# Performance work log

Measured on AMD Instinct MI355X. Metric: run time of the kernel, lower is better.

Reference implementation:

```python
import jax, jax.numpy as jnp
import numpy as np


def setup_inputs() -> dict:
    key = jax.random.key(0)
    k_x, k_pos, k_val, k_temp = jax.random.split(key, 4)
    B, T, D, N = 8, 2048, 512, 4096
    x = jax.random.normal(k_x, (B, T, D), dtype=jnp.float32)
    # module init: positions ~ N(0,1)*0.5, values ~ N(0,1)*0.02
    positions = jax.random.normal(k_pos, (N, D), dtype=jnp.float32) * 0.5
    values = jax.random.normal(k_val, (N, D), dtype=jnp.float32) * 0.02
    # 'trained' temperatures ~ U[4,6] so the RBF kernel does not underflow at D=512
    temperature = 4.0 + 2.0 * jax.random.uniform(k_temp, (N,), dtype=jnp.float32)
    # neuron_scale buffer at late-tide level (MAX_SCALE = 0.8)
    neuron_scale = jnp.full((N,), 0.8, dtype=jnp.float32)
    return {"x": x, "positions": positions, "values": values,
            "temperature": temperature, "neuron_scale": neuron_scale}


def reference(x, positions, values, temperature, neuron_scale):
    B, T, D = x.shape
    x_flat = x.reshape(-1, D)                                  # [M, D], M = B*T
    x_sq = jnp.sum(x_flat * x_flat, axis=-1, keepdims=True)    # [M, 1]
    p_sq = jnp.sum(positions * positions, axis=-1)             # [N]
    cross = x_flat @ positions.T                               # [M, N] GEMM
    dists = jnp.sqrt(jnp.maximum(x_sq + p_sq[None, :] - 2.0 * cross, 0.0))
    effective_temp = (jnp.abs(temperature) + 0.1) * neuron_scale  # [N]
    weights = jnp.exp(-dists / effective_temp[None, :])        # [M, N]
    weights = weights / (jnp.sum(weights, axis=-1, keepdims=True) + 1e-8)
    out = weights @ values                                     # [M, D] GEMM
    return out.reshape(B, T, D)
```

## Files before the change

kernel.cpp:

```cpp
#include <hip/hip_runtime.h>
#include <hip/hip_bf16.h>

typedef __attribute__((ext_vector_type(8))) short short8;
typedef __attribute__((ext_vector_type(4))) float f32x4;
typedef __attribute__((ext_vector_type(4))) unsigned short u16x4;

__device__ __forceinline__ unsigned short f2bf(float f) {
  union { float f; unsigned u; } v; v.f = f;
  unsigned r = v.u + 0x7fffu + ((v.u >> 16) & 1u);
  return (unsigned short)(r >> 16);
}

template <int EPI, int WM, int WN, int MI, int BK, int NBUF>
__global__ __launch_bounds__(512, 4) void rbf_gemm(
    const unsigned short* __restrict__ A, const unsigned short* __restrict__ Bt,
    int Ncols, int K,
    const float* __restrict__ xsq, const float* __restrict__ psq,
    const float* __restrict__ rtemp, unsigned short* __restrict__ Wout,
    float* __restrict__ part, int Mtot, const float* __restrict__ denin,
    float* __restrict__ outp, int row0, int ldOut) {
  constexpr int BM = WM * MI * 16;
  constexpr int BN = WN * 64;
  constexpr int CH = BK / 8;
  constexpr int CMASK = CH - 1;
  constexpr int AIT = BM * CH / 512;
  constexpr int BIT = BN * CH / 512;
  constexpr int LOADS = AIT + BIT;
  constexpr int DEPTH = NBUF - 1;
  constexpr int KS = BK / 32;
  constexpr int ASZ = BM * BK;
  constexpr int TSZ = (BM + BN) * BK;
  constexpr int BOUNCE = EPI == 1 ? BM * BN * 2 : BM * BN;
  constexpr int SELEMS = NBUF * TSZ > BOUNCE ? NBUF * TSZ : BOUNCE;
  __shared__ __align__(16) unsigned short smem[SELEMS];

  const int t = threadIdx.x;
  const int lane = t & 63, wid = t >> 6;
  const int wm = wid / WN, wn = wid % WN;
  const int lr = lane & 15, lg = lane >> 4;

  const int nb = Ncols / BN;
  const int nwg = gridDim.x;
  int swz = blockIdx.x;
  if ((nwg & 7) == 0) {
    int cpx = nwg >> 3;
    swz = (swz & 7) * cpx + (swz >> 3);
  }
  const int bm = swz / nb, bn = swz - bm * nb;

  const unsigned short* Ab = A + (size_t)bm * BM * K;
  const unsigned short* Bb = Bt + (size_t)bn * BN * K;

  const unsigned short* gA[AIT];
  const unsigned short* gB[BIT];
#pragma unroll
  for (int i = 0; i < AIT; ++i) {
    const int idx = i * 512 + t;
    const int r = idx / CH, c = idx & CMASK;
    gA[i] = Ab + (size_t)r * K + ((c ^ (r & CMASK)) << 3);
  }
#pragma unroll
  for (int i = 0; i < BIT; ++i) {
    const int idx = i * 512 + t;
    const int r = idx / CH, c = idx & CMASK;
    gB[i] = Bb + (size_t)r * K + ((c ^ (r & CMASK)) << 3);
  }
  const int dwave = wid << 9;

  int offA[MI][KS], offB[4][KS];
#pragma unroll
  for (int mi = 0; mi < MI; ++mi) {
    const int ar = wm * (MI * 16) + mi * 16 + lr;
#pragma unroll
    for (int ks = 0; ks < KS; ++ks)
      offA[mi][ks] = ar * BK + ((((ks << 2) | lg) ^ (ar & CMASK)) << 3);
  }
#pragma unroll
  for (int ni = 0; ni < 4; ++ni) {
    const int br = wn * 64 + ni * 16 + lr;
#pragma unroll
    for (int ks = 0; ks < KS; ++ks)
      offB[ni][ks] = ASZ + br * BK + ((((ks << 2) | lg) ^ (br & CMASK)) << 3);
  }

  f32x4 acc[MI][4];
#pragma unroll
  for (int i = 0; i < MI; ++i)
#pragma unroll
    for (int j = 0; j < 4; ++j) acc[i][j] = (f32x4){0.f, 0.f, 0.f, 0.f};

#define STAGE(step, bufi)                                                              \
  do {                                                                                 \
    const int ko = (step) * BK;                                                        \
    const int bo = (bufi) * TSZ;                                                       \
    _Pragma("unroll")                                                                  \
    for (int i = 0; i < AIT; ++i)                                                      \
      __builtin_amdgcn_global_load_lds(                                                \
          (const __attribute__((address_space(1))) void*)(gA[i] + ko),                 \
          (__attribute__((address_space(3))) void*)(smem + bo + i * 4096 + dwave),     \
          16, 0, 0);                                                                   \
    _Pragma("unroll")                                                                  \
    for (int i = 0; i < BIT; ++i)                                                      \
      __builtin_amdgcn_global_load_lds(                                                \
          (const __attribute__((address_space(1))) void*)(gB[i] + ko),                 \
          (__attribute__((address_space(3))) void*)(smem + bo + ASZ + i * 4096 + dwave), \
          16, 0, 0);                                                                   \
  } while (0)

  const int nsteps = K / BK;
#pragma unroll
  for (int p = 0; p < DEPTH; ++p)
    if (p < nsteps) STAGE(p, p);

  int bc = 0, bp = DEPTH % NBUF;
  for (int s = 0; s < nsteps; ++s) {
    if (s + DEPTH < nsteps) {
      STAGE(s + DEPTH, bp);
      asm volatile("s_waitcnt vmcnt(%0)" :: "i"(DEPTH * LOADS) : "memory");
    } else if (DEPTH >= 2 && s + 1 < nsteps) {
      asm volatile("s_waitcnt vmcnt(%0)" :: "i"(LOADS) : "memory");
    } else {
      asm volatile("s_waitcnt vmcnt(0)" ::: "memory");
    }
    __builtin_amdgcn_s_barrier();
    const unsigned short* sb = smem + bc * TSZ;
    __builtin_amdgcn_s_setprio(1);
#pragma unroll
    for (int ks = 0; ks < KS; ++ks) {
      short8 af[MI], bf[4];
#pragma unroll
      for (int mi = 0; mi < MI; ++mi) af[mi] = *(const short8*)&sb[offA[mi][ks]];
#pragma unroll
      for (int ni = 0; ni < 4; ++ni) bf[ni] = *(const short8*)&sb[offB[ni][ks]];
#pragma unroll
      for (int mi = 0; mi < MI; ++mi)
#pragma unroll
        for (int ni = 0; ni < 4; ++ni)
          acc[mi][ni] = __builtin_amdgcn_mfma_f32_16x16x32_bf16(af[mi], bf[ni],
                                                                acc[mi][ni], 0, 0, 0);
    }
    __builtin_amdgcn_s_setprio(0);
    asm volatile("s_waitcnt lgkmcnt(0)" ::: "memory");
    __builtin_amdgcn_s_barrier();
    bc = bc + 1 == NBUF ? 0 : bc + 1;
    bp = bp + 1 == NBUF ? 0 : bp + 1;
  }
#undef STAGE

  if (EPI == 0) {
    float ps[4], rt[4];
#pragma unroll
    for (int ni = 0; ni < 4; ++ni) {
      const int col = bn * BN + wn * 64 + ni * 16 + lr;
      ps[ni] = psq[col];
      rt[ni] = rtemp[col];
    }
    float* slice = part + (size_t)(bn * WN + wn) * Mtot;
#pragma unroll
    for (int mi = 0; mi < MI; ++mi) {
#pragma unroll
      for (int j = 0; j < 4; ++j) {
        const int lrow = wm * (MI * 16) + mi * 16 + lg * 4 + j;
        const int grow = row0 + bm * BM + lrow;
        const float xq = xsq[grow];
        float rsv = 0.f;
#pragma unroll
        for (int ni = 0; ni < 4; ++ni) {
          const int lcol = wn * 64 + ni * 16 + lr;
          float d2 = xq + ps[ni] - 2.0f * acc[mi][ni][j];
          float dist = __builtin_amdgcn_sqrtf(fmaxf(d2, 0.0f));
          float w = __builtin_amdgcn_exp2f(-dist * rt[ni]);
          smem[lrow * BN + (((lcol >> 3) ^ (lrow & 7)) << 3) + (lcol & 7)] = f2bf(w);
          rsv += w;
        }
        rsv += __shfl_xor(rsv, 1);
        rsv += __shfl_xor(rsv, 2);
        rsv += __shfl_xor(rsv, 4);
        rsv += __shfl_xor(rsv, 8);
        if (lr == 0) slice[grow] = rsv;
      }
    }
    __syncthreads();
    constexpr int HB = BN / 8;
#pragma unroll
    for (int i = 0; i < BM * BN / 8 / 512; ++i) {
      const int id = i * 512 + t;
      const int r = id / HB, h = id % HB;
      short8 v = *(const short8*)&smem[r * BN + ((h ^ (r & 7)) << 3)];
      *(short8*)&Wout[(size_t)(bm * BM + r) * ldOut + bn * BN + h * 8] = v;
    }
  } else {
    float* smemf = (float*)smem;
#pragma unroll
    for (int mi = 0; mi < MI; ++mi)
#pragma unroll
      for (int j = 0; j < 4; ++j) {
        const int lrow = wm * (MI * 16) + mi * 16 + lg * 4 + j;
#pragma unroll
        for (int ni = 0; ni < 4; ++ni) {
          const int lcol = wn * 64 + ni * 16 + lr;
          smemf[lrow * BN + (((lcol >> 2) ^ (lrow & 7)) << 2) + (lcol & 3)] =
              acc[mi][ni][j];
        }
      }
    __syncthreads();
    constexpr int HB4 = BN / 4;
#pragma unroll
    for (int i = 0; i < BM * BN / 4 / 512; ++i) {
      const int id = i * 512 + t;
      const int r = id / HB4, h = id % HB4;
      const int grow = row0 + bm * BM + r;
      const float rd = 1.0f / (denin[grow] + 1e-8f);
      f32x4 v = *(const f32x4*)&smemf[r * BN + ((h ^ (r & 7)) << 2)];
      v *= rd;
      __builtin_nontemporal_store(v,
          (f32x4*)&outp[(size_t)grow * ldOut + bn * BN + h * 4]);
    }
  }
}

__global__ void reduce_denom(const float* __restrict__ part, float* __restrict__ denom,
                             int Mtot, int row0, int S) {
  const int m = row0 + blockIdx.x * 128 + threadIdx.x;
  float s = 0.f;
  for (int i = 0; i < S; ++i) s += part[(size_t)i * Mtot + m];
  denom[m] = s;
}

__global__ void prep_rows(const float* __restrict__ in, unsigned short* __restrict__ outb,
                          float* __restrict__ sq, int D) {
  const int row = blockIdx.x;
  const int t = threadIdx.x;
  const float4 v = ((const float4*)(in + (size_t)row * D))[t];
  u16x4 o = {f2bf(v.x), f2bf(v.y), f2bf(v.z), f2bf(v.w)};
  *(u16x4*)(outb + (size_t)row * D + t * 4) = o;
  float s = v.x * v.x + v.y * v.y + v.z * v.z + v.w * v.w;
  for (int off = 32; off; off >>= 1) s += __shfl_xor(s, off);
  __shared__ float ws[16];
  if ((t & 63) == 0) ws[t >> 6] = s;
  __syncthreads();
  if (t == 0) {
    float tot = 0.f;
    const int nw = blockDim.x >> 6;
    for (int i = 0; i < nw; ++i) tot += ws[i];
    sq[row] = tot;
  }
}

__global__ void prep_scale(const float* __restrict__ tmp, const float* __restrict__ sc,
                           float* __restrict__ rtemp, int N) {
  const int i = blockIdx.x * blockDim.x + threadIdx.x;
  if (i < N) rtemp[i] = 1.4426950408889634f / ((fabsf(tmp[i]) + 0.1f) * sc[i]);
}

__global__ void prep_vT(const float* __restrict__ vals, unsigned short* __restrict__ vT,
                        int N, int D) {
  __shared__ float tile[32][33];
  const int nt = blockIdx.x, dt = blockIdx.y;
  const int tx = threadIdx.x, ty = threadIdx.y;
#pragma unroll
  for (int i = 0; i < 4; ++i) {
    int r = nt * 32 + ty + i * 8;
    tile[ty + i * 8][tx] = vals[(size_t)r * D + dt * 32 + tx];
  }
  __syncthreads();
#pragma unroll
  for (int i = 0; i < 4; ++i) {
    int d = dt * 32 + ty + i * 8;
    vT[(size_t)d * N + nt * 32 + tx] = f2bf(tile[tx][ty + i * 8]);
  }
}

extern "C" void kernel_launch(void* const* d_in, const int* in_sizes, int n_in,
                              void* d_out, int out_size, void* d_ws, size_t ws_size,
                              hipStream_t stream) {
  const float* x = (const float*)d_in[0];
  const float* pos = (const float*)d_in[1];
  const float* vals = (const float*)d_in[2];
  const float* temp = (const float*)d_in[3];
  const float* nsc = (const float*)d_in[4];
  float* out = (float*)d_out;

  const int N = in_sizes[3];
  const int D = in_sizes[1] / N;
  const int M = in_sizes[0] / D;
  const int S = 2 * (N / 128);

  char* ws = (char*)d_ws;
  size_t off = 0;
  auto alloc = [&](size_t bytes) {
    void* p = ws + off;
    off = (off + bytes + 255) & ~(size_t)255;
    return p;
  };
  unsigned short* xb = (unsigned short*)alloc((size_t)M * D * 2);
  unsigned short* pb = (unsigned short*)alloc((size_t)N * D * 2);
  unsigned short* vT = (unsigned short*)alloc((size_t)D * N * 2);
  float* xsq = (float*)alloc((size_t)M * 4);
  float* psq = (float*)alloc((size_t)N * 4);
  float* rtemp = (float*)alloc((size_t)N * 4);
  float* denom = (float*)alloc((size_t)M * 4);
  float* part = (float*)alloc((size_t)S * M * 4);

  size_t avail = ws_size > off ? ws_size - off : 0;
  long long mc_ll = (long long)(avail / ((size_t)N * 2));
  int Mc = (int)((mc_ll / 128) * 128);
  if (Mc > M) Mc = M;
  if (Mc < 128) Mc = 128;
  unsigned short* W = (unsigned short*)alloc((size_t)Mc * N * 2);

  prep_rows<<<M, D / 4, 0, stream>>>(x, xb, xsq, D);
  prep_rows<<<N, D / 4, 0, stream>>>(pos, pb, psq, D);
  prep_scale<<<(N + 255) / 256, 256, 0, stream>>>(temp, nsc, rtemp, N);
  dim3 tg(N / 32, D / 32);
  prep_vT<<<tg, dim3(32, 8), 0, stream>>>(vals, vT, N, D);

  for (int row0 = 0; row0 < M; row0 += Mc) {
    const int mc = (M - row0) < Mc ? (M - row0) : Mc;
    const int g1 = (mc / 128) * (N / 128);
    rbf_gemm<0, 4, 2, 2, 32, 3><<<g1, 512, 0, stream>>>(
        xb + (size_t)row0 * D, pb, N, D, xsq, psq, rtemp, W, part, M,
        nullptr, nullptr, row0, N);
    reduce_denom<<<mc / 128, 128, 0, stream>>>(part, denom, M, row0, S);
    const int g2 = (mc / 128) * (D / 256);
    rbf_gemm<1, 2, 4, 4, 64, 2><<<g2, 512, 0, stream>>>(
        W, vT, D, N, nullptr, nullptr, nullptr, nullptr,
        part, M, denom, out, row0, D);
  }
}
```

Measured before the change: 216.3 us.

## Parameterize GEMM thread count, retile first GEMM and reorder second-GEMM block mapping

Generalizes the templated GEMM so its thread count comes from the warp grid instead of a fixed 512. The first distance GEMM moves to 256 threads with 4 M-fragments per warp, BK=64 and double buffering. Block indexing for the second GEMM becomes column-major so consecutive workgroups share the same values tile and walk down rows. Occupancy hints drop to 2 blocks per CU. The aim is better per-warp reuse and fewer barriers per K step, at the cost of more registers per thread and shallower prefetch.

New measurement: 238.2 us. 1.1x slower.

```diff
diff --git a/kernel.cpp b/kernel.cpp
--- a/kernel.cpp
+++ b/kernel.cpp
@@ -12,19 +12,20 @@
 }
 
 template <int EPI, int WM, int WN, int MI, int BK, int NBUF>
-__global__ __launch_bounds__(512, 4) void rbf_gemm(
+__global__ __launch_bounds__(WM * WN * 64, 2) void rbf_gemm(
     const unsigned short* __restrict__ A, const unsigned short* __restrict__ Bt,
     int Ncols, int K,
     const float* __restrict__ xsq, const float* __restrict__ psq,
     const float* __restrict__ rtemp, unsigned short* __restrict__ Wout,
     float* __restrict__ part, int Mtot, const float* __restrict__ denin,
     float* __restrict__ outp, int row0, int ldOut) {
+  constexpr int NT = WM * WN * 64;
   constexpr int BM = WM * MI * 16;
   constexpr int BN = WN * 64;
   constexpr int CH = BK / 8;
   constexpr int CMASK = CH - 1;
-  constexpr int AIT = BM * CH / 512;
-  constexpr int BIT = BN * CH / 512;
+  constexpr int AIT = BM * CH / NT;
+  constexpr int BIT = BN * CH / NT;
   constexpr int LOADS = AIT + BIT;
   constexpr int DEPTH = NBUF - 1;
   constexpr int KS = BK / 32;
@@ -39,14 +40,24 @@
   const int wm = wid / WN, wn = wid % WN;
   const int lr = lane & 15, lg = lane >> 4;
 
-  const int nb = Ncols / BN;
-  const int nwg = gridDim.x;
-  int swz = blockIdx.x;
-  if ((nwg & 7) == 0) {
-    int cpx = nwg >> 3;
-    swz = (swz & 7) * cpx + (swz >> 3);
-  }
-  const int bm = swz / nb, bn = swz - bm * nb;
+  int bm, bn;
+  {
+    int swz = blockIdx.x;
+    if (EPI == 0) {
+      const int nb = Ncols / BN;
+      const int nwg = gridDim.x;
+      if ((nwg & 7) == 0) {
+        int cpx = nwg >> 3;
+        swz = (swz & 7) * cpx + (swz >> 3);
+      }
+      bm = swz / nb;
+      bn = swz - bm * nb;
+    } else {
+      const int nbm = gridDim.x / (Ncols / BN);
+      bm = swz % nbm;
+      bn = swz / nbm;
+    }
+  }
 
   const unsigned short* Ab = A + (size_t)bm * BM * K;
   const unsigned short* Bb = Bt + (size_t)bn * BN * K;
@@ -55,13 +66,13 @@
   const unsigned short* gB[BIT];
 #pragma unroll
   for (int i = 0; i < AIT; ++i) {
-    const int idx = i * 512 + t;
+    const int idx = i * NT + t;
     const int r = idx / CH, c = idx & CMASK;
     gA[i] = Ab + (size_t)r * K + ((c ^ (r & CMASK)) << 3);
   }
 #pragma unroll
   for (int i = 0; i < BIT; ++i) {
-    const int idx = i * 512 + t;
+    const int idx = i * NT + t;
     const int r = idx / CH, c = idx & CMASK;
     gB[i] = Bb + (size_t)r * K + ((c ^ (r & CMASK)) << 3);
   }
@@ -97,13 +108,13 @@
     for (int i = 0; i < AIT; ++i)                                                      \
       __builtin_amdgcn_global_load_lds(                                                \
           (const __attribute__((address_space(1))) void*)(gA[i] + ko),                 \
-          (__attribute__((address_space(3))) void*)(smem + bo + i * 4096 + dwave),     \
+          (__attribute__((address_space(3))) void*)(smem + bo + i * (NT * 8) + dwave), \
           16, 0, 0);                                                                   \
     _Pragma("unroll")                                                                  \
     for (int i = 0; i < BIT; ++i)                                                      \
       __builtin_amdgcn_global_load_lds(                                                \
           (const __attribute__((address_space(1))) void*)(gB[i] + ko),                 \
-          (__attribute__((address_space(3))) void*)(smem + bo + ASZ + i * 4096 + dwave), \
+          (__attribute__((address_space(3))) void*)(smem + bo + ASZ + i * (NT * 8) + dwave), \
           16, 0, 0);                                                                   \
   } while (0)
 
@@ -183,8 +194,8 @@
     __syncthreads();
     constexpr int HB = BN / 8;
 #pragma unroll
-    for (int i = 0; i < BM * BN / 8 / 512; ++i) {
-      const int id = i * 512 + t;
+    for (int i = 0; i < BM * BN / 8 / NT; ++i) {
+      const int id = i * NT + t;
       const int r = id / HB, h = id % HB;
       short8 v = *(const short8*)&smem[r * BN + ((h ^ (r & 7)) << 3)];
       *(short8*)&Wout[(size_t)(bm * BM + r) * ldOut + bn * BN + h * 8] = v;
@@ -206,8 +217,8 @@
     __syncthreads();
     constexpr int HB4 = BN / 4;
 #pragma unroll
-    for (int i = 0; i < BM * BN / 4 / 512; ++i) {
-      const int id = i * 512 + t;
+    for (int i = 0; i < BM * BN / 4 / NT; ++i) {
+      const int id = i * NT + t;
       const int r = id / HB4, h = id % HB4;
       const int grow = row0 + bm * BM + r;
       const float rd = 1.0f / (denin[grow] + 1e-8f);
@@ -318,7 +329,7 @@
   for (int row0 = 0; row0 < M; row0 += Mc) {
     const int mc = (M - row0) < Mc ? (M - row0) : Mc;
     const int g1 = (mc / 128) * (N / 128);
-    rbf_gemm<0, 4, 2, 2, 32, 3><<<g1, 512, 0, stream>>>(
+    rbf_gemm<0, 2, 2, 4, 64, 2><<<g1, 256, 0, stream>>>(
         xb + (size_t)row0 * D, pb, N, D, xsq, psq, rtemp, W, part, M,
         nullptr, nullptr, row0, N);
     reduce_denom<<<mc / 128, 128, 0, stream>>>(part, denom, M, row0, S);
```
